# Optimization experiments

Hardware: AMD Instinct MI355X
Metric: run time of the kernel (lower is better)

Reference implementation:

```python
import jax, jax.numpy as jnp
import numpy as np

H = 1024          # hidden_size
NH = 16           # num_attention_heads
HD = H // NH      # attention_head_size
EPS = 1e-12       # layer_norm_eps
NEG = jnp.finfo(jnp.float32).min


def setup_inputs() -> dict:
    key = jax.random.key(0)
    ks = jax.random.split(key, 12)
    B, S = 4, 2048
    sc = 1.0 / np.sqrt(H)
    return {
        "hidden_states": jax.random.normal(ks[0], (B, S, H), jnp.float32),
        "attention_mask": jnp.ones((B, S), jnp.float32),
        "Wq": jax.random.normal(ks[1], (H, H), jnp.float32) * sc,
        "bq": jnp.zeros((H,), jnp.float32),
        "Wk": jax.random.normal(ks[2], (H, H), jnp.float32) * sc,
        "bk": jnp.zeros((H,), jnp.float32),
        "Wv": jax.random.normal(ks[3], (H, H), jnp.float32) * sc,
        "bv": jnp.zeros((H,), jnp.float32),
        "Wo": jax.random.normal(ks[4], (H, H), jnp.float32) * sc,
        "bo": jnp.zeros((H,), jnp.float32),
        "ln_g": jnp.ones((H,), jnp.float32),
        "ln_b": jnp.zeros((H,), jnp.float32),
    }


def _split_heads(x):
    # (B, S, H) -> (B, NH, S, HD)
    B, S, _ = x.shape
    return x.reshape(B, S, NH, HD).transpose(0, 2, 1, 3)


def reference(hidden_states, attention_mask, Wq, bq, Wk, bk, Wv, bv, Wo, bo, ln_g, ln_b):
    q = _split_heads(hidden_states @ Wq + bq)
    k = _split_heads(hidden_states @ Wk + bk)
    v = _split_heads(hidden_states @ Wv + bv)

    # (B, NH, S, S)
    scores = jnp.einsum('bhqd,bhkd->bhqk', q, k) / jnp.sqrt(jnp.float32(HD))
    mask_add = (1.0 - attention_mask)[:, None, None, :] * NEG
    scores = scores + mask_add
    probs = jax.nn.softmax(scores, axis=-1)  # dropout is identity (eval / p=0)

    ctx = jnp.einsum('bhqk,bhkd->bhqd', probs, v)
    B, _, S, _ = ctx.shape
    ctx = ctx.transpose(0, 2, 1, 3).reshape(B, S, H)

    out = ctx @ Wo + bo
    x = out + hidden_states
    mu = jnp.mean(x, axis=-1, keepdims=True)
    var = jnp.var(x, axis=-1, keepdims=True)
    return (x - mu) * jax.lax.rsqrt(var + EPS) * ln_g + ln_b
```

## Files before the change

kernel.cpp:

```cpp
#include <hip/hip_runtime.h>
#include <stdint.h>

#define H_ 1024
#define NH_ 16
#define HD_ 64
#define B_ 4
#define S_ 2048
#define M_ (B_*S_)

typedef unsigned short u16;
typedef __attribute__((ext_vector_type(4))) unsigned short u16x4;
typedef __attribute__((ext_vector_type(8))) short bf16x8;
typedef __attribute__((ext_vector_type(4))) float f32x4;
typedef __attribute__((ext_vector_type(16))) float f32x16;
typedef __attribute__((ext_vector_type(4))) unsigned int u32x4;
typedef __attribute__((ext_vector_type(4))) int i32x4;

#define AS1 __attribute__((address_space(1)))
#define AS3 __attribute__((address_space(3)))

__device__ __forceinline__ void gload16(const void* g, void* l) {
  __builtin_amdgcn_global_load_lds((const AS1 void*)g, (AS3 void*)l, 16, 0, 0);
}

__device__ __forceinline__ u16 f2bf(float f) {
  union { float f; uint32_t u; } v; v.f = f;
  uint32_t u = v.u + 0x7FFFu + ((v.u >> 16) & 1u);
  return (u16)(u >> 16);
}

static __device__ __forceinline__ f32x4 mfma16(bf16x8 a, bf16x8 b, f32x4 c) {
  return __builtin_amdgcn_mfma_f32_16x16x32_bf16(a, b, c, 0, 0, 0);
}
static __device__ __forceinline__ f32x16 mfma32(bf16x8 a, bf16x8 b, f32x16 c) {
  return __builtin_amdgcn_mfma_f32_32x32x16_bf16(a, b, c, 0, 0, 0);
}

__device__ __forceinline__ int cvtpk(float lo, float hi) {
  int r;
  asm("v_cvt_pk_bf16_f32 %0, %1, %2" : "=v"(r) : "v"(lo), "v"(hi));
  return r;
}
__device__ __forceinline__ void plswap(int& a, int& b) {
  asm volatile("v_permlane32_swap_b32 %0, %1" : "+v"(a), "+v"(b));
}
#if __has_builtin(__builtin_amdgcn_exp2f)
#define EXP2F __builtin_amdgcn_exp2f
#else
#define EXP2F exp2f
#endif

__device__ __forceinline__ int xcd_swz(int bid, int nwg) {
  return (bid & 7) * (nwg >> 3) + (bid >> 3);
}


__global__ __launch_bounds__(256) void prep_kernel(const float* __restrict__ in, u16* __restrict__ out,
                                                   const float* __restrict__ mask, float* __restrict__ madd_g,
                                                   uint32_t* __restrict__ nzbits,
                                                   const float* __restrict__ Wq, const float* __restrict__ Wk,
                                                   const float* __restrict__ Wv, const float* __restrict__ Wo,
                                                   u16* __restrict__ wt) {
  __shared__ float tile[64][65];
  const int bid = blockIdx.x, t = threadIdx.x;
  if (bid < 4096) {
    int i = bid * 256 + t;
    const f32x4* p = (const f32x4*)in;
    f32x4 a = p[2*i], b = p[2*i+1];
    u32x4 o;
    o.x = (uint32_t)f2bf(a.x) | ((uint32_t)f2bf(a.y) << 16);
    o.y = (uint32_t)f2bf(a.z) | ((uint32_t)f2bf(a.w) << 16);
    o.z = (uint32_t)f2bf(b.x) | ((uint32_t)f2bf(b.y) << 16);
    o.w = (uint32_t)f2bf(b.z) | ((uint32_t)f2bf(b.w) << 16);
    ((u32x4*)out)[i] = o;
  } else if (bid < 4100) {
    const int mb = bid - 4096;
    int i = mb * 256 + t;
    f32x4 a = ((const f32x4*)mask)[2*i], b4 = ((const f32x4*)mask)[2*i+1];
    f32x4 ma, mb4;
    ma.x = (1.0f - a.x) * -3.0e38f;  ma.y = (1.0f - a.y) * -3.0e38f;
    ma.z = (1.0f - a.z) * -3.0e38f;  ma.w = (1.0f - a.w) * -3.0e38f;
    mb4.x = (1.0f - b4.x) * -3.0e38f; mb4.y = (1.0f - b4.y) * -3.0e38f;
    mb4.z = (1.0f - b4.z) * -3.0e38f; mb4.w = (1.0f - b4.w) * -3.0e38f;
    ((f32x4*)madd_g)[2*i] = ma;  ((f32x4*)madd_g)[2*i+1] = mb4;
    if (mb == 0) {
      if (t < B_) nzbits[t] = 0u;
      __syncthreads();
      if (t < B_*32) {
        int b = t >> 5, kt = t & 31;
        const float* mrow = mask + (size_t)b * S_ + kt*64;
        uint32_t nz = 0;
        for (int c = 0; c < 64; ++c) nz |= (mrow[c] != 1.0f) ? 1u : 0u;
        if (nz) atomicOr(&nzbits[b], 1u << kt);
      }
    }
  } else {
    const int w = bid - 4100;
    const int p = w >> 8, ti = w & 255, tr = ti >> 4, tc = ti & 15;
    const float* W = (p == 0) ? Wq : (p == 1) ? Wk : (p == 2) ? Wv : Wo;
#pragma unroll
    for (int it = 0; it < 16; ++it) {
      int idx = it * 256 + t, r = idx >> 6, c = idx & 63;
      tile[r][c] = W[(size_t)(tr*64 + r) * H_ + tc*64 + c];
    }
    __syncthreads();
    u16* outp = wt + (size_t)p * H_ * H_;
#pragma unroll
    for (int it = 0; it < 16; ++it) {
      int idx = it * 256 + t, r = idx >> 6, c = idx & 63;
      outp[(size_t)(tc*64 + r) * H_ + tr*64 + c] = f2bf(tile[c][r]);
    }
  }
}


__device__ __forceinline__ void gemm_tile(const u16* __restrict__ A, const u16* __restrict__ Bt,
                                          int m0, int n0, u16* As, u16* Bs, f32x4 acc[4][4]) {
  const int tid = threadIdx.x;
  const int lane = tid & 63, wave = tid >> 6;
  const int wr = wave >> 1, wc = wave & 1;
  const int l15 = lane & 15, l4 = lane >> 4;
  const int r0 = tid >> 2, c0 = (tid & 3) * 8;
  const u16* Ap0 = A + (size_t)(m0 + r0) * H_ + c0;
  const u16* Ap1 = A + (size_t)(m0 + 64 + r0) * H_ + c0;
  const u16* Bp0 = Bt + (size_t)(n0 + r0) * H_ + c0;
  const u16* Bp1 = Bt + (size_t)(n0 + 64 + r0) * H_ + c0;
#define GSTAGE(bb, k0) do { \
    gload16(Ap0 + (k0), As + (bb)*4096 + (size_t)tid * 8); \
    gload16(Ap1 + (k0), As + (bb)*4096 + 2048 + (size_t)tid * 8); \
    gload16(Bp0 + (k0), Bs + (bb)*4096 + (size_t)tid * 8); \
    gload16(Bp1 + (k0), Bs + (bb)*4096 + 2048 + (size_t)tid * 8); \
  } while (0)
  GSTAGE(0, 0);
  for (int kt = 0; kt < 32; ++kt) {
    const int cur = kt & 1;
    const int nk = ((kt + 1) & 31) * 32;
    GSTAGE(cur ^ 1, nk);
    asm volatile("s_waitcnt vmcnt(4)\n\ts_barrier" ::: "memory");
    const u16* Ab = As + cur*4096;
    const u16* Bb = Bs + cur*4096;
    bf16x8 afr[4], bfr[4];
#pragma unroll
    for (int m = 0; m < 4; ++m) afr[m] = *(const bf16x8*)&Ab[(wr*64 + m*16 + l15) * 32 + l4*8];
#pragma unroll
    for (int n = 0; n < 4; ++n) bfr[n] = *(const bf16x8*)&Bb[(wc*64 + n*16 + l15) * 32 + l4*8];
#pragma unroll
    for (int m = 0; m < 4; ++m)
#pragma unroll
      for (int n = 0; n < 4; ++n)
        acc[m][n] = mfma16(afr[m], bfr[n], acc[m][n]);
    asm volatile("s_barrier" ::: "memory");
  }
  asm volatile("s_waitcnt vmcnt(0)" ::: "memory");
#undef GSTAGE
}

__global__ __launch_bounds__(256) void gemm_qkv_kernel(const u16* __restrict__ hs16, const u16* __restrict__ wt,
                                                       const float* __restrict__ bq, const float* __restrict__ bk,
                                                       const float* __restrict__ bv, u16* __restrict__ qkv16) {
  __shared__ __align__(16) u16 As[2*128*32], Bs[2*128*32];
  f32x4 acc[4][4] = {};
  const int lg = xcd_swz(blockIdx.x, 1536);
  const int m0 = (lg / 24) * 128, n0 = (lg % 24) * 128;
  gemm_tile(hs16, wt, m0, n0, As, Bs, acc);
  const int tid = threadIdx.x, lane = tid & 63, wave = tid >> 6;
  const int wr = wave >> 1, wc = wave & 1, l15 = lane & 15, l4 = lane >> 4;
  const int p = n0 >> 10;
  const float* bias = (p == 0) ? bq : (p == 1) ? bk : bv;
  const float qsc = (p == 0) ? 0.18033688f : 1.0f;
  u16* base = qkv16 + (size_t)p * ((size_t)B_*NH_*S_*HD_);
  if (p == 2) {
    const int b = m0 >> 11;
#pragma unroll
    for (int n = 0; n < 4; ++n) {
      int ncol = (n0 & 1023) + wc*64 + n*16 + l15;
      int h = ncol >> 6, d = ncol & 63;
      float bsv = bias[ncol];
#pragma unroll
      for (int m = 0; m < 4; ++m) {
        int s0 = (m0 & 2047) + wr*64 + m*16 + l4*4;
        u16x4 pk;
#pragma unroll
        for (int r = 0; r < 4; ++r) pk[r] = f2bf(acc[m][n][r] + bsv);
        *(u16x4*)(base + (((size_t)b*NH_ + h)*HD_ + d)*S_ + s0) = pk;
      }
    }
  } else {
#pragma unroll
    for (int n = 0; n < 4; ++n) {
      int ncol = (n0 & 1023) + wc*64 + n*16 + l15;
      int h = ncol >> 6, d = ncol & 63;
      float bsv = bias[ncol];
#pragma unroll
      for (int m = 0; m < 4; ++m) {
#pragma unroll
        for (int r = 0; r < 4; ++r) {
          int row = m0 + wr*64 + m*16 + l4*4 + r;
          int b = row >> 11, s = row & 2047;
          base[(((size_t)b*NH_ + h)*S_ + s)*HD_ + d] = f2bf((acc[m][n][r] + bsv) * qsc);
        }
      }
    }
  }
}

__global__ __launch_bounds__(256) void gemm_out_kernel(const u16* __restrict__ ctx16, const u16* __restrict__ wo,
                                                       const float* __restrict__ bo, const float* __restrict__ hs,
                                                       float* __restrict__ xout) {
  __shared__ __align__(16) u16 As[2*128*32], Bs[2*128*32];
  f32x4 acc[4][4] = {};
  const int lg = xcd_swz(blockIdx.x, 512);
  const int m0 = (lg / 8) * 128, n0 = (lg % 8) * 128;
  gemm_tile(ctx16, wo, m0, n0, As, Bs, acc);
  const int tid = threadIdx.x, lane = tid & 63, wave = tid >> 6;
  const int wr = wave >> 1, wc = wave & 1, l15 = lane & 15, l4 = lane >> 4;
#pragma unroll
  for (int n = 0; n < 4; ++n) {
    int col = n0 + wc*64 + n*16 + l15;
    float bsv = bo[col];
#pragma unroll
    for (int m = 0; m < 4; ++m) {
#pragma unroll
      for (int r = 0; r < 4; ++r) {
        int row = m0 + wr*64 + m*16 + l4*4 + r;
        size_t off = (size_t)row * H_ + col;
        xout[off] = acc[m][n][r] + bsv + hs[off];
      }
    }
  }
}


__global__ __launch_bounds__(256, 2) void attn_kernel(const u16* __restrict__ q_, const u16* __restrict__ k_,
                                                      const u16* __restrict__ vt_, const float* __restrict__ madd_g,
                                                      const uint32_t* __restrict__ nzbits,
                                                      u16* __restrict__ ctx16) {
  __shared__ __align__(16) u16 Ks[2][64*64], Vs[2][64*64];
  const int lgid = xcd_swz(blockIdx.x, 512);
  const int qb = lgid & 7, bh = lgid >> 3, h = bh & 15, b = bh >> 4;
  const int tid = threadIdx.x, lane = tid & 63, wave = tid >> 6;
  const int l31 = lane & 31, hi = lane >> 5;
  const size_t headoff = ((size_t)b * NH_ + h) * ((size_t)S_ * HD_);
  const u16* Q  = q_ + headoff;
  const u16* K  = k_ + headoff;
  const u16* Vt = vt_ + headoff;
  const uint32_t nzb = nzbits[b];
  const int qbase = qb*256 + wave*64;
  bf16x8 qfA[4], qfB[4];
#pragma unroll
  for (int st = 0; st < 4; ++st) {
    qfA[st] = *(const bf16x8*)(Q + (size_t)(qbase + l31) * HD_ + st*16 + hi*8);
    qfB[st] = *(const bf16x8*)(Q + (size_t)(qbase + 32 + l31) * HD_ + st*16 + hi*8);
  }
  union { i32x4 i; bf16x8 hv; } uo;
  uo.i = (i32x4){0x3F803F80, 0x3F803F80, 0x3F803F80, 0x3F803F80};
  const bf16x8 ones = uo.hv;
  f32x16 O00 = {}, O01 = {}, O10 = {}, O11 = {};
  f32x16 LA = {}, LB = {};
  const int srow = tid >> 3, sch = tid & 7;
  const int gch = sch ^ (srow & 7);
  const int swzA = l31 & 7;

#define STAGE(bb, kt) do { \
    const u16* Kt_ = K + (size_t)(kt) * 64 * HD_; \
    _Pragma("unroll") \
    for (int c = 0; c < 2; ++c) { \
      int row = c*32 + srow; \
      gload16(Kt_ + (size_t)row * HD_ + gch*8, &Ks[bb][c*2048 + (size_t)tid*8]); \
      gload16(Vt + (size_t)row * S_ + (kt)*64 + gch*8, &Vs[bb][c*2048 + (size_t)tid*8]); \
    } \
  } while (0)

  STAGE(0, 0);
  __syncthreads();

  for (int kt = 0; kt < 32; ++kt) {
    const int cur = kt & 1;
    const int nxt = (kt + 1) & 31;
    STAGE(cur ^ 1, nxt);
    asm volatile("s_waitcnt vmcnt(4)\n\ts_barrier" ::: "memory");
    f32x16 sA0 = {}, sA1 = {}, sB0 = {}, sB1 = {};
    __builtin_amdgcn_s_setprio(1);
#pragma unroll
    for (int st = 0; st < 4; ++st) {
      const int kch = ((2*st + hi) ^ swzA) * 8;
      bf16x8 kf0 = *(const bf16x8*)&Ks[cur][l31*64 + kch];
      bf16x8 kf1 = *(const bf16x8*)&Ks[cur][(32 + l31)*64 + kch];
      sA0 = mfma32(kf0, qfA[st], sA0);
      sA1 = mfma32(kf1, qfA[st], sA1);
      sB0 = mfma32(kf0, qfB[st], sB0);
      sB1 = mfma32(kf1, qfB[st], sB1);
    }
    __builtin_amdgcn_s_setprio(0);
    if ((nzb >> kt) & 1u) {
#pragma unroll
      for (int t = 0; t < 2; ++t) {
        f32x16& sa = t ? sA1 : sA0;
        f32x16& sb = t ? sB1 : sB0;
#pragma unroll
        for (int bq = 0; bq < 4; ++bq) {
          f32x4 md = *(const f32x4*)(madd_g + (size_t)b * S_ + kt*64 + t*32 + bq*8 + hi*4);
#pragma unroll
          for (int a = 0; a < 4; ++a) { sa[bq*4 + a] += md[a]; sb[bq*4 + a] += md[a]; }
        }
      }
    }
#pragma unroll
    for (int r = 0; r < 16; ++r) sA0[r] = EXP2F(sA0[r]);
#pragma unroll
    for (int r = 0; r < 16; ++r) sA1[r] = EXP2F(sA1[r]);
#pragma unroll
    for (int r = 0; r < 16; ++r) sB0[r] = EXP2F(sB0[r]);
#pragma unroll
    for (int r = 0; r < 16; ++r) sB1[r] = EXP2F(sB1[r]);
    __builtin_amdgcn_s_setprio(1);
#pragma unroll
    for (int ks = 0; ks < 4; ++ks) {
      const f32x16& sa = (ks < 2) ? sA0 : sA1;
      const f32x16& sb = (ks < 2) ? sB0 : sB1;
      const int p = ks & 1;
      int pa0 = cvtpk(sa[8*p+0], sa[8*p+1]);
      int pa1 = cvtpk(sa[8*p+2], sa[8*p+3]);
      int pa2 = cvtpk(sa[8*p+4], sa[8*p+5]);
      int pa3 = cvtpk(sa[8*p+6], sa[8*p+7]);
      plswap(pa0, pa2); plswap(pa1, pa3);
      union { i32x4 i; bf16x8 hv; } ua; ua.i = (i32x4){pa0, pa1, pa2, pa3};
      int pb0 = cvtpk(sb[8*p+0], sb[8*p+1]);
      int pb1 = cvtpk(sb[8*p+2], sb[8*p+3]);
      int pb2 = cvtpk(sb[8*p+4], sb[8*p+5]);
      int pb3 = cvtpk(sb[8*p+6], sb[8*p+7]);
      plswap(pb0, pb2); plswap(pb1, pb3);
      union { i32x4 i; bf16x8 hv; } ub; ub.i = (i32x4){pb0, pb1, pb2, pb3};
      const int vch = ((2*ks + hi) ^ swzA) * 8;
      bf16x8 vb0 = *(const bf16x8*)&Vs[cur][l31*64 + vch];
      bf16x8 vb1 = *(const bf16x8*)&Vs[cur][(32 + l31)*64 + vch];
      O00 = mfma32(ua.hv, vb0, O00);
      O01 = mfma32(ua.hv, vb1, O01);
      LA  = mfma32(ua.hv, ones,    LA);
      O10 = mfma32(ub.hv, vb0, O10);
      O11 = mfma32(ub.hv, vb1, O11);
      LB  = mfma32(ub.hv, ones,    LB);
    }
    __builtin_amdgcn_s_setprio(0);
    asm volatile("s_barrier" ::: "memory");
  }
  asm volatile("s_waitcnt vmcnt(0)" ::: "memory");
#pragma unroll
  for (int bq = 0; bq < 4; ++bq) {
#pragma unroll
    for (int a = 0; a < 4; ++a) {
      int ql = 8*bq + 4*hi + a, r = bq*4 + a;
      float iA = 1.0f / LA[r], iB = 1.0f / LB[r];
      int sA_ = qbase + ql;
      size_t ob0 = ((size_t)(b * S_ + sA_) * NH_ + h) * HD_;
      ctx16[ob0 + l31]      = f2bf(O00[r] * iA);
      ctx16[ob0 + 32 + l31] = f2bf(O01[r] * iA);
      int sB_ = qbase + 32 + ql;
      size_t ob1 = ((size_t)(b * S_ + sB_) * NH_ + h) * HD_;
      ctx16[ob1 + l31]      = f2bf(O10[r] * iB);
      ctx16[ob1 + 32 + l31] = f2bf(O11[r] * iB);
    }
  }
#undef STAGE
}


__global__ __launch_bounds__(256) void ln_kernel(float* __restrict__ x, const float* __restrict__ g,
                                                 const float* __restrict__ bb) {
  const int row = blockIdx.x, t = threadIdx.x;
  float* xr = x + (size_t)row * H_;
  f32x4 v = ((const f32x4*)xr)[t];
  float s = v.x + v.y + v.z + v.w;
  float s2 = v.x*v.x + v.y*v.y + v.z*v.z + v.w*v.w;
#pragma unroll
  for (int o = 1; o < 64; o <<= 1) { s += __shfl_xor(s, o, 64); s2 += __shfl_xor(s2, o, 64); }
  __shared__ float red[8];
  const int wave = t >> 6, lane = t & 63;
  if (lane == 0) { red[wave] = s; red[4 + wave] = s2; }
  __syncthreads();
  s = red[0] + red[1] + red[2] + red[3];
  s2 = red[4] + red[5] + red[6] + red[7];
  const float mu = s * (1.0f / H_);
  const float var = s2 * (1.0f / H_) - mu * mu;
  const float rs = rsqrtf(var + 1e-12f);
  f32x4 gg = ((const f32x4*)g)[t], bb4 = ((const f32x4*)bb)[t];
  f32x4 o;
  o.x = (v.x - mu) * rs * gg.x + bb4.x;
  o.y = (v.y - mu) * rs * gg.y + bb4.y;
  o.z = (v.z - mu) * rs * gg.z + bb4.z;
  o.w = (v.w - mu) * rs * gg.w + bb4.w;
  ((f32x4*)xr)[t] = o;
}


extern "C" void kernel_launch(void* const* d_in, const int* in_sizes, int n_in,
                              void* d_out, int out_size, void* d_ws, size_t ws_size,
                              hipStream_t stream) {
  (void)in_sizes; (void)n_in; (void)out_size; (void)ws_size;
  const float* hs   = (const float*)d_in[0];
  const float* mask = (const float*)d_in[1];
  const float* Wq = (const float*)d_in[2];
  const float* bq = (const float*)d_in[3];
  const float* Wk = (const float*)d_in[4];
  const float* bk = (const float*)d_in[5];
  const float* Wv = (const float*)d_in[6];
  const float* bv = (const float*)d_in[7];
  const float* Wo = (const float*)d_in[8];
  const float* bo = (const float*)d_in[9];
  const float* lg = (const float*)d_in[10];
  const float* lb = (const float*)d_in[11];
  float* out = (float*)d_out;

  uint8_t* w = (uint8_t*)d_ws;
  u16* hs16  = (u16*)w;
  u16* wt16  = (u16*)(w + ((size_t)16 << 20));
  u16* qkv16 = (u16*)(w + ((size_t)24 << 20));
  u16* ctx16 = (u16*)(w + ((size_t)72 << 20));
  float* madd_g = (float*)(w + ((size_t)88 << 20));
  uint32_t* nzbits = (uint32_t*)(w + ((size_t)88 << 20) + 32768);

  const size_t psz = (size_t)B_*NH_*S_*HD_;
  prep_kernel<<<dim3(5124), dim3(256), 0, stream>>>(hs, hs16, mask, madd_g, nzbits,
                                                    Wq, Wk, Wv, Wo, wt16);
  gemm_qkv_kernel<<<dim3(1536), dim3(256), 0, stream>>>(hs16, wt16, bq, bk, bv, qkv16);
  attn_kernel<<<dim3(512), dim3(256), 0, stream>>>(qkv16, qkv16 + psz, qkv16 + 2*psz, madd_g, nzbits, ctx16);
  gemm_out_kernel<<<dim3(512), dim3(256), 0, stream>>>(ctx16, wt16 + (size_t)3*H_*H_, bo, hs, out);
  ln_kernel<<<dim3(M_), dim3(256), 0, stream>>>(out, lg, lb);
}
```

Baseline: 203.2 us.

## Halve attention block size and replace ones-MFMA row sums with VALU reductions

The attention kernel now runs 1024 blocks of 128 threads (2 waves, 128 queries each) instead of 512 blocks of 256 threads, and K/V tile staging is redistributed to 4 loads per thread. The softmax denominator is no longer computed with extra MFMAs against a ones vector. Each lane sums its exp values and combines across lane halves with a permlane swap, then the reciprocals are broadcast through a small shared buffer. This removes a third of the PV-stage MFMAs and spreads work over more blocks, but each block's K/V tile loads are amortized over fewer queries, so global/L2 traffic per query roughly doubles.

```diff
diff --git a/kernel.cpp b/kernel.cpp
--- a/kernel.cpp
+++ b/kernel.cpp
@@ -231,13 +231,14 @@
 }
 
 
-__global__ __launch_bounds__(256, 2) void attn_kernel(const u16* __restrict__ q_, const u16* __restrict__ k_,
-                                                      const u16* __restrict__ vt_, const float* __restrict__ madd_g,
-                                                      const uint32_t* __restrict__ nzbits,
-                                                      u16* __restrict__ ctx16) {
+__global__ __launch_bounds__(128) void attn_kernel(const u16* __restrict__ q_, const u16* __restrict__ k_,
+                                                   const u16* __restrict__ vt_, const float* __restrict__ madd_g,
+                                                   const uint32_t* __restrict__ nzbits,
+                                                   u16* __restrict__ ctx16) {
   __shared__ __align__(16) u16 Ks[2][64*64], Vs[2][64*64];
-  const int lgid = xcd_swz(blockIdx.x, 512);
-  const int qb = lgid & 7, bh = lgid >> 3, h = bh & 15, b = bh >> 4;
+  __shared__ __align__(16) float Sc[2][64];
+  const int lgid = xcd_swz(blockIdx.x, 1024);
+  const int qb = lgid & 15, bh = lgid >> 4, h = bh & 15, b = bh >> 4;
   const int tid = threadIdx.x, lane = tid & 63, wave = tid >> 6;
   const int l31 = lane & 31, hi = lane >> 5;
   const size_t headoff = ((size_t)b * NH_ + h) * ((size_t)S_ * HD_);
@@ -245,29 +246,26 @@
   const u16* K  = k_ + headoff;
   const u16* Vt = vt_ + headoff;
   const uint32_t nzb = nzbits[b];
-  const int qbase = qb*256 + wave*64;
+  const int qbase = qb*128 + wave*64;
   bf16x8 qfA[4], qfB[4];
 #pragma unroll
   for (int st = 0; st < 4; ++st) {
     qfA[st] = *(const bf16x8*)(Q + (size_t)(qbase + l31) * HD_ + st*16 + hi*8);
     qfB[st] = *(const bf16x8*)(Q + (size_t)(qbase + 32 + l31) * HD_ + st*16 + hi*8);
   }
-  union { i32x4 i; bf16x8 hv; } uo;
-  uo.i = (i32x4){0x3F803F80, 0x3F803F80, 0x3F803F80, 0x3F803F80};
-  const bf16x8 ones = uo.hv;
   f32x16 O00 = {}, O01 = {}, O10 = {}, O11 = {};
-  f32x16 LA = {}, LB = {};
+  float lA = 0.f, lB = 0.f;
   const int srow = tid >> 3, sch = tid & 7;
-  const int gch = sch ^ (srow & 7);
   const int swzA = l31 & 7;
 
 #define STAGE(bb, kt) do { \
     const u16* Kt_ = K + (size_t)(kt) * 64 * HD_; \
     _Pragma("unroll") \
-    for (int c = 0; c < 2; ++c) { \
-      int row = c*32 + srow; \
-      gload16(Kt_ + (size_t)row * HD_ + gch*8, &Ks[bb][c*2048 + (size_t)tid*8]); \
-      gload16(Vt + (size_t)row * S_ + (kt)*64 + gch*8, &Vs[bb][c*2048 + (size_t)tid*8]); \
+    for (int c = 0; c < 4; ++c) { \
+      int row = c*16 + srow; \
+      int gch = sch ^ (row & 7); \
+      gload16(Kt_ + (size_t)row * HD_ + gch*8, &Ks[bb][c*1024 + (size_t)tid*8]); \
+      gload16(Vt + (size_t)row * S_ + (kt)*64 + gch*8, &Vs[bb][c*1024 + (size_t)tid*8]); \
     } \
   } while (0)
 
@@ -278,7 +276,7 @@
     const int cur = kt & 1;
     const int nxt = (kt + 1) & 31;
     STAGE(cur ^ 1, nxt);
-    asm volatile("s_waitcnt vmcnt(4)\n\ts_barrier" ::: "memory");
+    asm volatile("s_waitcnt vmcnt(8)\n\ts_barrier" ::: "memory");
     f32x16 sA0 = {}, sA1 = {}, sB0 = {}, sB1 = {};
     __builtin_amdgcn_s_setprio(1);
 #pragma unroll
@@ -313,6 +311,27 @@
     for (int r = 0; r < 16; ++r) sB0[r] = EXP2F(sB0[r]);
 #pragma unroll
     for (int r = 0; r < 16; ++r) sB1[r] = EXP2F(sB1[r]);
+    {
+      float v[16];
+#pragma unroll
+      for (int r = 0; r < 16; ++r) v[r] = sA0[r] + sA1[r];
+#pragma unroll
+      for (int r = 0; r < 8; ++r) v[r] += v[r+8];
+#pragma unroll
+      for (int r = 0; r < 4; ++r) v[r] += v[r+4];
+      float rs_ = (v[0] + v[1]) + (v[2] + v[3]);
+      int a0 = __float_as_int(rs_), b0 = a0; plswap(a0, b0);
+      lA += __int_as_float(a0) + __int_as_float(b0);
+#pragma unroll
+      for (int r = 0; r < 16; ++r) v[r] = sB0[r] + sB1[r];
+#pragma unroll
+      for (int r = 0; r < 8; ++r) v[r] += v[r+8];
+#pragma unroll
+      for (int r = 0; r < 4; ++r) v[r] += v[r+4];
+      rs_ = (v[0] + v[1]) + (v[2] + v[3]);
+      int a1 = __float_as_int(rs_), b1 = a1; plswap(a1, b1);
+      lB += __int_as_float(a1) + __int_as_float(b1);
+    }
     __builtin_amdgcn_s_setprio(1);
 #pragma unroll
     for (int ks = 0; ks < 4; ++ks) {
@@ -336,29 +355,30 @@
       bf16x8 vb1 = *(const bf16x8*)&Vs[cur][(32 + l31)*64 + vch];
       O00 = mfma32(ua.hv, vb0, O00);
       O01 = mfma32(ua.hv, vb1, O01);
-      LA  = mfma32(ua.hv, ones,    LA);
       O10 = mfma32(ub.hv, vb0, O10);
       O11 = mfma32(ub.hv, vb1, O11);
-      LB  = mfma32(ub.hv, ones,    LB);
     }
     __builtin_amdgcn_s_setprio(0);
     asm volatile("s_barrier" ::: "memory");
   }
   asm volatile("s_waitcnt vmcnt(0)" ::: "memory");
+  Sc[wave][l31]      = 1.0f / lA;
+  Sc[wave][32 + l31] = 1.0f / lB;
 #pragma unroll
   for (int bq = 0; bq < 4; ++bq) {
+    f32x4 i0 = *(const f32x4*)&Sc[wave][bq*8 + hi*4];
+    f32x4 i1 = *(const f32x4*)&Sc[wave][32 + bq*8 + hi*4];
 #pragma unroll
     for (int a = 0; a < 4; ++a) {
       int ql = 8*bq + 4*hi + a, r = bq*4 + a;
-      float iA = 1.0f / LA[r], iB = 1.0f / LB[r];
       int sA_ = qbase + ql;
       size_t ob0 = ((size_t)(b * S_ + sA_) * NH_ + h) * HD_;
-      ctx16[ob0 + l31]      = f2bf(O00[r] * iA);
-      ctx16[ob0 + 32 + l31] = f2bf(O01[r] * iA);
+      ctx16[ob0 + l31]      = f2bf(O00[r] * i0[a]);
+      ctx16[ob0 + 32 + l31] = f2bf(O01[r] * i0[a]);
       int sB_ = qbase + 32 + ql;
       size_t ob1 = ((size_t)(b * S_ + sB_) * NH_ + h) * HD_;
-      ctx16[ob1 + l31]      = f2bf(O10[r] * iB);
-      ctx16[ob1 + 32 + l31] = f2bf(O11[r] * iB);
+      ctx16[ob1 + l31]      = f2bf(O10[r] * i1[a]);
+      ctx16[ob1 + 32 + l31] = f2bf(O11[r] * i1[a]);
     }
   }
 #undef STAGE
@@ -423,7 +443,7 @@
   prep_kernel<<<dim3(5124), dim3(256), 0, stream>>>(hs, hs16, mask, madd_g, nzbits,
                                                     Wq, Wk, Wv, Wo, wt16);
   gemm_qkv_kernel<<<dim3(1536), dim3(256), 0, stream>>>(hs16, wt16, bq, bk, bv, qkv16);
-  attn_kernel<<<dim3(512), dim3(256), 0, stream>>>(qkv16, qkv16 + psz, qkv16 + 2*psz, madd_g, nzbits, ctx16);
+  attn_kernel<<<dim3(1024), dim3(128), 0, stream>>>(qkv16, qkv16 + psz, qkv16 + 2*psz, madd_g, nzbits, ctx16);
   gemm_out_kernel<<<dim3(512), dim3(256), 0, stream>>>(ctx16, wt16 + (size_t)3*H_*H_, bo, hs, out);
   ln_kernel<<<dim3(M_), dim3(256), 0, stream>>>(out, lg, lb);
 }
```

New measurement: 250.6 us. 23.3% more time.
